# Kernel optimization log

Hardware: AMD Instinct MI355X
Metric: run time of the kernel (lower is better)

The kernel has to match this reference:

```python
import jax, jax.numpy as jnp
import numpy as np

B, T, N, C = 32, 64, 1000, 8
HG, HL, OUT, E = 16, 256, 24, 16000


def setup_inputs() -> dict:
    key = jax.random.key(0)
    ks = jax.random.split(key, 12)
    inp = {
        'x': jax.random.normal(ks[0], (B, T, N, C), jnp.float32),
        'edge_index': jax.random.randint(ks[1], (2, E), 0, N, jnp.int32),
        'edge_weight': jax.random.uniform(ks[2], (E,), jnp.float32),
        # GCNConv params (linear without bias applied before propagate, bias added after)
        'W_gcn': jax.random.normal(ks[3], (C, HG), jnp.float32) * (1.0 / np.sqrt(C)),
        'b_gcn': jnp.zeros((HG,), jnp.float32),
        # single-layer torch LSTM params (gate order i,f,g,o)
        'W_ih': jax.random.normal(ks[4], (4 * HL, N * HG), jnp.float32) * (1.0 / np.sqrt(N * HG)),
        'W_hh': jax.random.normal(ks[5], (4 * HL, HL), jnp.float32) * (1.0 / np.sqrt(HL)),
        'b_ih': jnp.zeros((4 * HL,), jnp.float32),
        'b_hh': jnp.zeros((4 * HL,), jnp.float32),
        'W_proj': jax.random.normal(ks[6], (OUT, HL), jnp.float32) * (1.0 / np.sqrt(HL)),
        'b_proj': jnp.zeros((OUT,), jnp.float32),
    }
    return inp


def reference(x, edge_index, edge_weight, W_gcn, b_gcn, W_ih, W_hh, b_ih, b_hh, W_proj, b_proj):
    b, t, n, c = x.shape
    hg = W_gcn.shape[1]
    row, col = edge_index[0], edge_index[1]

    # --- GCNConv normalization (gcn_norm with self-loops, fill_value=1) ---
    # Edges index only nodes 0..N-1 of the flattened [b*n] node axis, i.e. batch 0
    # (faithful to the original code's batched-flatten bug). Nodes of batch>0 get
    # degree 1 (self-loop only).
    deg0 = jax.ops.segment_sum(edge_weight, col, num_segments=n) + 1.0  # [n]
    dis = deg0 ** -0.5
    norm = dis[row] * edge_weight * dis[col]                            # [E]

    xw = jnp.einsum('btnc,ch->btnh', x, W_gcn)                          # [b,t,n,hg]

    # self-loop contribution: 1/deg for batch 0, identity (deg=1) for batch>0
    inv_deg = jnp.ones((b, n), x.dtype).at[0].set(1.0 / deg0)
    out = xw * inv_deg[:, None, :, None]

    # neighbor aggregation (only batch 0 receives messages)
    msg = norm[None, :, None] * xw[0][:, row, :]                        # [t,E,hg]
    agg0 = jnp.zeros((t, n, hg), x.dtype).at[:, col, :].add(msg)        # [t,n,hg]
    h_gcn = out.at[0].add(agg0) + b_gcn                                 # [b,t,n,hg]

    seq = h_gcn.reshape(b, t, n * hg)

    # --- single-layer LSTM (batch_first), torch gate order i,f,g,o ---
    hl = W_hh.shape[1]
    bias = b_ih + b_hh

    def step(carry, xt):
        h, cc = carry
        gates = xt @ W_ih.T + h @ W_hh.T + bias
        i, f, g, o = jnp.split(gates, 4, axis=-1)
        i, f, o = jax.nn.sigmoid(i), jax.nn.sigmoid(f), jax.nn.sigmoid(o)
        g = jnp.tanh(g)
        cc = f * cc + i * g
        h = o * jnp.tanh(cc)
        return (h, cc), None

    h0 = jnp.zeros((b, hl), x.dtype)
    (h_last, _), _ = jax.lax.scan(step, (h0, h0), seq.transpose(1, 0, 2))

    return h_last @ W_proj.T + b_proj
```

## Files before the change

kernel.cpp:

```cpp
#include <hip/hip_runtime.h>
#include <stdint.h>

#define Bz 32
#define Tz 64
#define Nz 1000
#define Cz 8
#define HGz 16
#define HLz 256
#define OUTz 24
#define Ez 16000
#define K2z 8000
#define Mz 2048
#define G4z 1024
#define NSz 8

using half8  = __attribute__((ext_vector_type(8))) _Float16;
using half4  = __attribute__((ext_vector_type(4))) _Float16;
using floatx4 = __attribute__((ext_vector_type(4))) float;

#define SENT 0x7E7E7E7E7E7E7E7EULL

static const size_t OFF_IDEG   = 4096;
static const size_t OFF_CNT    = 73728;
static const size_t OFF_ROFF   = 77824;
static const size_t OFF_CSRS   = 86016;
static const size_t OFF_CSRW   = 151552;
static const size_t OFF_HLAST  = 217088;
static const size_t OFF_PRE16T = 249856;
static const size_t OFF_WHH16  = 4444160;
static const size_t OFF_HX     = 4968448;
static const size_t OFF_BGC    = 6037504;
static const size_t OFF_XT     = 6041600;
static const size_t OFF_WC     = 38809600;
static const size_t OFF_PRES   = 55193600;
static const size_t WS_NEED    = 88748032;

__device__ __forceinline__ void gl_lds16(const void* g, void* l) {
  __builtin_amdgcn_global_load_lds(
      (__attribute__((address_space(1))) void*)(void*)g,
      (__attribute__((address_space(3))) void*)l, 16, 0, 0);
}

__device__ __forceinline__ float sigm(float x) { return 1.0f / (1.0f + __expf(-x)); }
__device__ __forceinline__ float tanhh(float x) { return 1.0f - 2.0f / (__expf(2.0f * x) + 1.0f); }

__global__ void __launch_bounds__(1024) k_prep(const int* __restrict__ ei,
                                               const float* __restrict__ ew,
                                               float* __restrict__ ideg,
                                               int* __restrict__ cntg,
                                               int* __restrict__ roffg,
                                               int* __restrict__ csrs,
                                               float* __restrict__ csrw) {
  __shared__ float disS[1024];
  __shared__ int   cntS[1024];
  __shared__ int   curS[1024];
  __shared__ int   scanS[1024];
  int tid = threadIdx.x;
  disS[tid] = 1.0f;
  cntS[tid] = 0;
  __syncthreads();
  for (int e = tid; e < Ez; e += 1024) {
    int col = ei[Ez + e];
    atomicAdd(&disS[col], ew[e]);
    atomicAdd(&cntS[col], 1);
  }
  __syncthreads();
  float d = disS[tid];
  float dis = 1.0f / sqrtf(d);
  if (tid < Nz) ideg[tid] = 1.0f / d;
  __syncthreads();
  disS[tid] = dis;
  int v0 = cntS[tid];
  scanS[tid] = v0;
  __syncthreads();
  for (int off = 1; off < 1024; off <<= 1) {
    int v = (tid >= off) ? scanS[tid - off] : 0;
    __syncthreads();
    scanS[tid] += v;
    __syncthreads();
  }
  int excl = scanS[tid] - v0;
  roffg[tid] = excl;
  cntg[tid] = v0;
  curS[tid] = excl;
  __syncthreads();
  for (int e = tid; e < Ez; e += 1024) {
    int row = ei[e], col = ei[Ez + e];
    int p = atomicAdd(&curS[col], 1);
    csrs[p] = row;
    csrw[p] = disS[row] * ew[e] * disS[col];
  }
}

__global__ void __launch_bounds__(256) k_fold(const float* __restrict__ Wih,
                                              const float* __restrict__ Wg,
                                              const float* __restrict__ bg,
                                              _Float16* __restrict__ wc,
                                              float* __restrict__ bgc,
                                              const float* __restrict__ Whh,
                                              _Float16* __restrict__ whh16) {
  __shared__ float wgs[Cz * HGz];
  __shared__ float bgs[HGz];
  __shared__ float red[256];
  int tid = threadIdx.x;
  int j = blockIdx.x;
  if (j >= 1024) {
    size_t i = (size_t)(j - 1024) * 256 + tid;
    float4 a = ((const float4*)Whh)[i * 2];
    float4 b = ((const float4*)Whh)[i * 2 + 1];
    half8 h;
    h[0] = (_Float16)a.x; h[1] = (_Float16)a.y; h[2] = (_Float16)a.z; h[3] = (_Float16)a.w;
    h[4] = (_Float16)b.x; h[5] = (_Float16)b.y; h[6] = (_Float16)b.z; h[7] = (_Float16)b.w;
    ((half8*)whh16)[i] = h;
    return;
  }
  if (tid < Cz * HGz) wgs[tid] = Wg[tid];
  if (tid < HGz) bgs[tid] = bg[tid];
  __syncthreads();
  const float* row = Wih + (size_t)j * (Nz * HGz);
  float bacc = 0.f;
  for (int n = tid; n < Nz; n += 256) {
    const float* p = row + n * HGz;
    float w[16];
    float4 v0 = *(const float4*)p, v1 = *(const float4*)(p + 4);
    float4 v2 = *(const float4*)(p + 8), v3 = *(const float4*)(p + 12);
    w[0]=v0.x; w[1]=v0.y; w[2]=v0.z; w[3]=v0.w;
    w[4]=v1.x; w[5]=v1.y; w[6]=v1.z; w[7]=v1.w;
    w[8]=v2.x; w[9]=v2.y; w[10]=v2.z; w[11]=v2.w;
    w[12]=v3.x; w[13]=v3.y; w[14]=v3.z; w[15]=v3.w;
    half8 o;
#pragma unroll
    for (int c = 0; c < Cz; ++c) {
      float s = 0.f;
#pragma unroll
      for (int h = 0; h < HGz; ++h) s += w[h] * wgs[c * HGz + h];
      o[c] = (_Float16)s;
    }
#pragma unroll
    for (int h = 0; h < HGz; ++h) bacc += w[h] * bgs[h];
    *(half8*)(wc + (size_t)j * K2z + n * Cz) = o;
  }
  red[tid] = bacc;
  __syncthreads();
  for (int off = 128; off > 0; off >>= 1) {
    if (tid < off) red[tid] += red[tid + off];
    __syncthreads();
  }
  if (tid == 0) bgc[j] = red[0];
}

__global__ void k_xt(const float* __restrict__ x, const float* __restrict__ ideg,
                     const int* __restrict__ roff, const int* __restrict__ cnt,
                     const int* __restrict__ csrs, const float* __restrict__ csrw,
                     _Float16* __restrict__ xt) {
  if (blockIdx.x >= 250) {
    size_t i = (size_t)(blockIdx.x - 250) * 256 + threadIdx.x;
    const float* src = x + (size_t)Tz * K2z;
    _Float16* dst = xt + (size_t)Tz * K2z;
    float4 a = ((const float4*)src)[i * 2];
    float4 b = ((const float4*)src)[i * 2 + 1];
    half8 h;
    h[0] = (_Float16)a.x; h[1] = (_Float16)a.y; h[2] = (_Float16)a.z; h[3] = (_Float16)a.w;
    h[4] = (_Float16)b.x; h[5] = (_Float16)b.y; h[6] = (_Float16)b.z; h[7] = (_Float16)b.w;
    ((half8*)dst)[i] = h;
    return;
  }
  int g = blockIdx.x * 256 + threadIdx.x;
  if (g >= Tz * Nz) return;
  int t = g / Nz, n = g % Nz;
  const float* xp = x + (size_t)g * Cz;
  float4 a = *(const float4*)xp, b = *(const float4*)(xp + 4);
  float id = ideg[n];
  float s[8] = {id*a.x, id*a.y, id*a.z, id*a.w, id*b.x, id*b.y, id*b.z, id*b.w};
  int i0 = roff[n], nc = cnt[n];
  for (int i = i0; i < i0 + nc; ++i) {
    int src = csrs[i];
    float wv = csrw[i];
    const float* q = x + ((size_t)t * Nz + src) * Cz;
    float4 u = *(const float4*)q, v = *(const float4*)(q + 4);
    s[0] += wv * u.x; s[1] += wv * u.y; s[2] += wv * u.z; s[3] += wv * u.w;
    s[4] += wv * v.x; s[5] += wv * v.y; s[6] += wv * v.z; s[7] += wv * v.w;
  }
  half8 h;
#pragma unroll
  for (int c = 0; c < 8; ++c) h[c] = (_Float16)s[c];
  *(half8*)(xt + (size_t)t * K2z + n * Cz) = h;
}

__global__ void __launch_bounds__(256) k_gemm(const _Float16* __restrict__ A,
                                              const _Float16* __restrict__ Bm,
                                              _Float16* __restrict__ Cp) {
  __shared__ _Float16 As[128 * 32];
  __shared__ _Float16 Bs[128 * 32];
  const int tid = threadIdx.x;
  const int lane = tid & 63;
  const int wave = tid >> 6;
  const int wm = wave & 1, wn = wave >> 1;
  const int quad = lane >> 4, l15 = lane & 15;
  const size_t tm = (size_t)blockIdx.x * 128;
  const size_t tn = (size_t)blockIdx.y * 128;
  const int k0 = blockIdx.z * 1024;
  const int iters = (blockIdx.z < 7) ? 32 : 26;
  _Float16* Cz_ = Cp + (size_t)blockIdx.z * Mz * G4z;
  const int srow = tid >> 2;
  const int skk = (tid & 3) * 8;
  const _Float16* gA0 = A + (tm + srow) * (size_t)K2z + k0 + skk;
  const _Float16* gA1 = gA0 + 64 * (size_t)K2z;
  const _Float16* gB0 = Bm + (tn + srow) * (size_t)K2z + k0 + skk;
  const _Float16* gB1 = gB0 + 64 * (size_t)K2z;
  _Float16* lA0 = &As[tid * 8];
  _Float16* lA1 = &As[2048 + tid * 8];
  _Float16* lB0 = &Bs[tid * 8];
  _Float16* lB1 = &Bs[2048 + tid * 8];
  floatx4 acc[4][4] = {};
  for (int kt = 0; kt < iters; ++kt) {
    __syncthreads();
    gl_lds16(gA0, lA0);
    gl_lds16(gA1, lA1);
    gl_lds16(gB0, lB0);
    gl_lds16(gB1, lB1);
    gA0 += 32; gA1 += 32; gB0 += 32; gB1 += 32;
    __syncthreads();
    half8 af[4], bf[4];
#pragma unroll
    for (int i = 0; i < 4; ++i)
      af[i] = *(const half8*)&As[(wm * 64 + i * 16 + l15) * 32 + quad * 8];
#pragma unroll
    for (int i = 0; i < 4; ++i)
      bf[i] = *(const half8*)&Bs[(wn * 64 + i * 16 + l15) * 32 + quad * 8];
#pragma unroll
    for (int mi = 0; mi < 4; ++mi)
#pragma unroll
      for (int ni = 0; ni < 4; ++ni)
        acc[mi][ni] = __builtin_amdgcn_mfma_f32_16x16x32_f16(af[mi], bf[ni], acc[mi][ni], 0, 0, 0);
  }
#pragma unroll
  for (int mi = 0; mi < 4; ++mi)
#pragma unroll
    for (int ni = 0; ni < 4; ++ni) {
      size_t r0 = tm + wm * 64 + mi * 16 + quad * 4;
      size_t cc = tn + wn * 64 + ni * 16 + l15;
#pragma unroll
      for (int q = 0; q < 4; ++q) Cz_[(r0 + q) * G4z + cc] = (_Float16)acc[mi][ni][q];
    }
}

__global__ void k_reduce(const _Float16* __restrict__ preS, const float* __restrict__ bih,
                         const float* __restrict__ bhh, const float* __restrict__ bgc,
                         _Float16* __restrict__ preT) {
  int t = blockIdx.x;
  int j = blockIdx.y * 256 + threadIdx.x;
  float bias = bih[j] + bhh[j] + bgc[j];
  float v[32];
#pragma unroll
  for (int b = 0; b < 32; ++b) v[b] = bias;
  for (int s = 0; s < NSz; ++s) {
    const _Float16* base = preS + (size_t)s * Mz * G4z;
#pragma unroll
    for (int b = 0; b < 32; ++b)
      v[b] += (float)base[((size_t)b * Tz + t) * G4z + j];
  }
  half8 h[4];
#pragma unroll
  for (int i = 0; i < 32; ++i) ((_Float16*)h)[i] = (_Float16)v[i];
  half8* op = (half8*)(preT + ((size_t)t * G4z + j) * Bz);
#pragma unroll
  for (int i = 0; i < 4; ++i) op[i] = h[i];
}

__global__ void __launch_bounds__(256) k_lstm4(const _Float16* __restrict__ Whh16,
                                               const _Float16* __restrict__ preT,
                                               unsigned long long* __restrict__ hx,
                                               float* __restrict__ hlast) {
  __shared__ _Float16 Ws[256 * 264];
  __shared__ _Float16 hs[2][16 * 264];
  const int tid = threadIdx.x;
  const int d   = blockIdx.x >> 2;
  const int ws_ = blockIdx.x & 3;
  const int wv = tid >> 6;
  const int lane = tid & 63;
  const int quad = lane >> 4, l15 = lane & 15;

  for (int i = tid; i < 2 * 16 * 264; i += 256) ((_Float16*)hs)[i] = (_Float16)0.f;
#pragma unroll
  for (int rr = 0; rr < 2; ++rr) {
    int rp = (tid >> 1) + rr * 128;
    int g = rp >> 6, hl64 = rp & 63;
    int grow = g * 256 + ws_ * 64 + hl64;
    const half8* src = (const half8*)(Whh16 + (size_t)grow * HLz + (tid & 1) * 128);
    half8* dst = (half8*)&Ws[rp * 264 + (tid & 1) * 128];
#pragma unroll
    for (int u = 0; u < 16; ++u) dst[u] = src[u];
  }
  float cst[4] = {0.f, 0.f, 0.f, 0.f};
  const int hlG = ws_ * 64 + wv * 16 + l15;
  __syncthreads();

  for (int t = 0; t < Tz; ++t) {
    half4 pq[4];
    if (quad == 0) {
#pragma unroll
      for (int g = 0; g < 4; ++g)
        pq[g] = *(const half4*)(preT + ((size_t)t * G4z + g * HLz + hlG) * Bz + d * 4);
    }
    if (t > 0) {
      const unsigned long long* hsrc = hx + ((size_t)d * 65 + t) * 256;
      unsigned long long u;
      while ((u = __hip_atomic_load(hsrc + tid, __ATOMIC_RELAXED,
                                    __HIP_MEMORY_SCOPE_AGENT)) == SENT)
        __builtin_amdgcn_s_sleep(1);
      half4 hv = __builtin_bit_cast(half4, u);
      _Float16* hb = &hs[t & 1][0];
#pragma unroll
      for (int q = 0; q < 4; ++q) hb[q * 264 + tid] = hv[q];
    }
    __syncthreads();
    floatx4 acc[4] = {};
    const _Float16* hrow = &hs[t & 1][0];
#pragma unroll
    for (int kt = 0; kt < 8; ++kt) {
      half8 a = *(const half8*)&hrow[l15 * 264 + kt * 32 + quad * 8];
#pragma unroll
      for (int g = 0; g < 4; ++g) {
        half8 b = *(const half8*)&Ws[(g * 64 + wv * 16 + l15) * 264 + kt * 32 + quad * 8];
        acc[g] = __builtin_amdgcn_mfma_f32_16x16x32_f16(a, b, acc[g], 0, 0, 0);
      }
    }
    if (quad == 0) {
      half4 o;
#pragma unroll
      for (int q = 0; q < 4; ++q) {
        float gi = acc[0][q] + (float)pq[0][q];
        float gf = acc[1][q] + (float)pq[1][q];
        float gg = acc[2][q] + (float)pq[2][q];
        float go = acc[3][q] + (float)pq[3][q];
        float iv = sigm(gi), fv = sigm(gf), gv = tanhh(gg), ov = sigm(go);
        float cn = fv * cst[q] + iv * gv;
        cst[q] = cn;
        float hn = ov * tanhh(cn);
        o[q] = (_Float16)hn;
        if (t == Tz - 1) hlast[(size_t)(d * 4 + q) * HLz + hlG] = hn;
      }
      if (t < Tz - 1) {
        __hip_atomic_store(hx + ((size_t)d * 65 + t + 1) * 256 + hlG,
                           __builtin_bit_cast(unsigned long long, o),
                           __ATOMIC_RELAXED, __HIP_MEMORY_SCOPE_AGENT);
      }
    }
  }
}

__global__ void k_proj(const float* __restrict__ hlast, const float* __restrict__ Wp,
                       const float* __restrict__ bp, float* __restrict__ out) {
  int idx = blockIdx.x * 256 + threadIdx.x;
  if (idx >= Bz * OUTz) return;
  int b = idx / OUTz, o = idx % OUTz;
  const float* h = hlast + (size_t)b * HLz;
  const float* wr = Wp + (size_t)o * HLz;
  float s = 0.f;
  for (int k = 0; k < HLz; k += 4) {
    float4 hv = *(const float4*)&h[k];
    float4 wv = *(const float4*)&wr[k];
    s += hv.x * wv.x + hv.y * wv.y + hv.z * wv.z + hv.w * wv.w;
  }
  out[idx] = s + bp[o];
}

extern "C" void kernel_launch(void* const* d_in, const int* in_sizes, int n_in,
                              void* d_out, int out_size, void* d_ws, size_t ws_size,
                              hipStream_t stream) {
  const float* x   = (const float*)d_in[0];
  const int*   ei  = (const int*)d_in[1];
  const float* ew  = (const float*)d_in[2];
  const float* Wg  = (const float*)d_in[3];
  const float* bg  = (const float*)d_in[4];
  const float* Wih = (const float*)d_in[5];
  const float* Whh = (const float*)d_in[6];
  const float* bih = (const float*)d_in[7];
  const float* bhh = (const float*)d_in[8];
  const float* Wp  = (const float*)d_in[9];
  const float* bp  = (const float*)d_in[10];
  float* out = (float*)d_out;
  char* ws = (char*)d_ws;
  if (ws_size < WS_NEED) return;

  float* ideg  = (float*)(ws + OFF_IDEG);
  int*   cnt   = (int*)(ws + OFF_CNT);
  int*   roff  = (int*)(ws + OFF_ROFF);
  int*   csrs  = (int*)(ws + OFF_CSRS);
  float* csrw  = (float*)(ws + OFF_CSRW);
  float* hlast = (float*)(ws + OFF_HLAST);
  _Float16* preT  = (_Float16*)(ws + OFF_PRE16T);
  _Float16* whh16 = (_Float16*)(ws + OFF_WHH16);
  unsigned long long* hx = (unsigned long long*)(ws + OFF_HX);
  float* bgc   = (float*)(ws + OFF_BGC);
  _Float16* xt    = (_Float16*)(ws + OFF_XT);
  _Float16* wc    = (_Float16*)(ws + OFF_WC);
  _Float16* preS  = (_Float16*)(ws + OFF_PRES);

  hipMemsetAsync(ws + OFF_HX, 0x7E, (size_t)8 * 65 * 256 * 8, stream);

  k_prep<<<1, 1024, 0, stream>>>(ei, ew, ideg, cnt, roff, csrs, csrw);
  k_fold<<<1152, 256, 0, stream>>>(Wih, Wg, bg, wc, bgc, Whh, whh16);
  k_xt<<<8000, 256, 0, stream>>>(x, ideg, roff, cnt, csrs, csrw, xt);
  k_gemm<<<dim3(16, 8, NSz), 256, 0, stream>>>(xt, wc, preS);
  k_reduce<<<dim3(Tz, 4), 256, 0, stream>>>(preS, bih, bhh, bgc, preT);
  k_lstm4<<<32, 256, 0, stream>>>(whh16, preT, hx, hlast);
  k_proj<<<3, 256, 0, stream>>>(hlast, Wp, bp, out);
}
```

Baseline: 456.7 us.

## Split LSTM recurrence across block pairs with half-K overlap and register-held weights

Replaces the 32-block LSTM kernel (4 blocks per 4-batch group, all exchanging h via global memory) with pairs of 512-thread blocks, each covering 16 batch rows and half the hidden units. Each block multiplies its own local half of h before it polls for the partner's half, so part of the MFMA work overlaps the cross-block wait. Half of the W_hh gate tiles are kept in registers to cut LDS traffic. Blocks are spread so only 4 of 16 do work, and each step now needs two block barriers and larger per-block LDS use.

```diff
diff --git a/kernel.cpp b/kernel.cpp
--- a/kernel.cpp
+++ b/kernel.cpp
@@ -268,85 +268,124 @@
   for (int i = 0; i < 4; ++i) op[i] = h[i];
 }
 
-__global__ void __launch_bounds__(256) k_lstm4(const _Float16* __restrict__ Whh16,
+template <int KB>
+__device__ __forceinline__ void mfma_phase(const _Float16* hrow,
+                                           const _Float16* wb0,
+                                           const _Float16* wb1,
+                                           const half8 (&wreg)[2][8],
+                                           floatx4 (&acc)[4]) {
+#pragma unroll
+  for (int kk = 0; kk < 4; ++kk) {
+    const int kt = KB + kk;
+    half8 a  = *(const half8*)(hrow + kt * 32);
+    half8 b0 = *(const half8*)(wb0 + kt * 32);
+    half8 b1 = *(const half8*)(wb1 + kt * 32);
+    acc[0] = __builtin_amdgcn_mfma_f32_16x16x32_f16(a, b0, acc[0], 0, 0, 0);
+    acc[1] = __builtin_amdgcn_mfma_f32_16x16x32_f16(a, b1, acc[1], 0, 0, 0);
+    acc[2] = __builtin_amdgcn_mfma_f32_16x16x32_f16(a, wreg[0][kt], acc[2], 0, 0, 0);
+    acc[3] = __builtin_amdgcn_mfma_f32_16x16x32_f16(a, wreg[1][kt], acc[3], 0, 0, 0);
+  }
+}
+
+__global__ void __launch_bounds__(512) k_lstm2(const _Float16* __restrict__ Whh16,
                                                const _Float16* __restrict__ preT,
                                                unsigned long long* __restrict__ hx,
                                                float* __restrict__ hlast) {
-  __shared__ _Float16 Ws[256 * 264];
-  __shared__ _Float16 hs[2][16 * 264];
+  const int sub = blockIdx.x & 7;
+  if (sub > 1) return;
+  const int bg = sub;
+  const int hh = blockIdx.x >> 3;
+
+  __shared__ _Float16 Ws[8 * 2 * 16 * 264];
+  __shared__ _Float16 hb[2 * 16 * 264];
+
   const int tid = threadIdx.x;
-  const int d   = blockIdx.x >> 2;
-  const int ws_ = blockIdx.x & 3;
-  const int wv = tid >> 6;
+  const int w = tid >> 6;
   const int lane = tid & 63;
   const int quad = lane >> 4, l15 = lane & 15;
 
-  for (int i = tid; i < 2 * 16 * 264; i += 256) ((_Float16*)hs)[i] = (_Float16)0.f;
-#pragma unroll
-  for (int rr = 0; rr < 2; ++rr) {
-    int rp = (tid >> 1) + rr * 128;
-    int g = rp >> 6, hl64 = rp & 63;
-    int grow = g * 256 + ws_ * 64 + hl64;
-    const half8* src = (const half8*)(Whh16 + (size_t)grow * HLz + (tid & 1) * 128);
-    half8* dst = (half8*)&Ws[rp * 264 + (tid & 1) * 128];
-#pragma unroll
-    for (int u = 0; u < 16; ++u) dst[u] = src[u];
-  }
+  for (int i = tid; i < 2 * 16 * 264; i += 512) hb[i] = (_Float16)0.f;
+
+  for (int i = tid; i < 256 * 32; i += 512) {
+    int lr = i >> 5, u = i & 31;
+    int g = lr >> 7, rr = lr & 127;
+    int ww = rr >> 4, r = rr & 15;
+    int grow = g * 256 + hh * 128 + rr;
+    *(half8*)&Ws[(((ww * 2 + g) * 16 + r) * 264) + u * 8] =
+        *(const half8*)(Whh16 + (size_t)grow * 256 + u * 8);
+  }
+  half8 wreg[2][8];
+#pragma unroll
+  for (int g = 0; g < 2; ++g) {
+    const _Float16* src = Whh16 + ((size_t)(g + 2) * 256 + hh * 128 + w * 16 + l15) * 256 + quad * 8;
+#pragma unroll
+    for (int kt = 0; kt < 8; ++kt) wreg[g][kt] = *(const half8*)(src + kt * 32);
+  }
+
+  const int hlL = w * 16 + l15;
+  const int hlG = hh * 128 + hlL;
+  unsigned long long* pubBase = hx + ((size_t)bg * 64 * 2 + hh) * 512 + (size_t)hlL * 4 + quad;
+  const unsigned long long* polBase = hx + ((size_t)bg * 64 * 2 + (hh ^ 1)) * 512 + tid;
+
+  const _Float16* wb0 = &Ws[((w * 2 + 0) * 16 + l15) * 264 + quad * 8];
+  const _Float16* wb1 = &Ws[((w * 2 + 1) * 16 + l15) * 264 + quad * 8];
+
   float cst[4] = {0.f, 0.f, 0.f, 0.f};
-  const int hlG = ws_ * 64 + wv * 16 + l15;
   __syncthreads();
 
   for (int t = 0; t < Tz; ++t) {
+    const int p = t & 1;
     half4 pq[4];
-    if (quad == 0) {
-#pragma unroll
-      for (int g = 0; g < 4; ++g)
-        pq[g] = *(const half4*)(preT + ((size_t)t * G4z + g * HLz + hlG) * Bz + d * 4);
-    }
+    const _Float16* pT = preT + (size_t)t * (G4z * Bz) + bg * 16 + quad * 4;
+#pragma unroll
+    for (int g = 0; g < 4; ++g)
+      pq[g] = *(const half4*)(pT + (size_t)(g * 256 + hlG) * Bz);
+
+    floatx4 acc[4] = {};
+    const _Float16* hrow = &hb[p * (16 * 264) + l15 * 264 + quad * 8];
+
+    if (hh == 0) mfma_phase<0>(hrow, wb0, wb1, wreg, acc);
+    else         mfma_phase<4>(hrow, wb0, wb1, wreg, acc);
+
     if (t > 0) {
-      const unsigned long long* hsrc = hx + ((size_t)d * 65 + t) * 256;
+      const unsigned long long* src = polBase + (size_t)t * 1024;
       unsigned long long u;
-      while ((u = __hip_atomic_load(hsrc + tid, __ATOMIC_RELAXED,
-                                    __HIP_MEMORY_SCOPE_AGENT)) == SENT)
+      while ((u = __hip_atomic_load(src, __ATOMIC_RELAXED, __HIP_MEMORY_SCOPE_AGENT)) == SENT)
         __builtin_amdgcn_s_sleep(1);
       half4 hv = __builtin_bit_cast(half4, u);
-      _Float16* hb = &hs[t & 1][0];
-#pragma unroll
-      for (int q = 0; q < 4; ++q) hb[q * 264 + tid] = hv[q];
+      const int phl = tid >> 2, pbh = tid & 3;
+      _Float16* dst = &hb[p * (16 * 264) + (pbh * 4) * 264 + ((hh ^ 1) * 128 + phl)];
+#pragma unroll
+      for (int q = 0; q < 4; ++q) dst[q * 264] = hv[q];
     }
     __syncthreads();
-    floatx4 acc[4] = {};
-    const _Float16* hrow = &hs[t & 1][0];
-#pragma unroll
-    for (int kt = 0; kt < 8; ++kt) {
-      half8 a = *(const half8*)&hrow[l15 * 264 + kt * 32 + quad * 8];
-#pragma unroll
-      for (int g = 0; g < 4; ++g) {
-        half8 b = *(const half8*)&Ws[(g * 64 + wv * 16 + l15) * 264 + kt * 32 + quad * 8];
-        acc[g] = __builtin_amdgcn_mfma_f32_16x16x32_f16(a, b, acc[g], 0, 0, 0);
-      }
+
+    if (hh == 0) mfma_phase<4>(hrow, wb0, wb1, wreg, acc);
+    else         mfma_phase<0>(hrow, wb0, wb1, wreg, acc);
+
+    half4 o4;
+#pragma unroll
+    for (int q = 0; q < 4; ++q) {
+      float gi = acc[0][q] + (float)pq[0][q];
+      float gf = acc[1][q] + (float)pq[1][q];
+      float gg = acc[2][q] + (float)pq[2][q];
+      float go = acc[3][q] + (float)pq[3][q];
+      float iv = sigm(gi), fv = sigm(gf), gv = tanhh(gg), ov = sigm(go);
+      float cn = fv * cst[q] + iv * gv;
+      cst[q] = cn;
+      float hn = ov * tanhh(cn);
+      o4[q] = (_Float16)hn;
+      if (t == Tz - 1) hlast[(size_t)(bg * 16 + quad * 4 + q) * HLz + hlG] = hn;
     }
-    if (quad == 0) {
-      half4 o;
-#pragma unroll
-      for (int q = 0; q < 4; ++q) {
-        float gi = acc[0][q] + (float)pq[0][q];
-        float gf = acc[1][q] + (float)pq[1][q];
-        float gg = acc[2][q] + (float)pq[2][q];
-        float go = acc[3][q] + (float)pq[3][q];
-        float iv = sigm(gi), fv = sigm(gf), gv = tanhh(gg), ov = sigm(go);
-        float cn = fv * cst[q] + iv * gv;
-        cst[q] = cn;
-        float hn = ov * tanhh(cn);
-        o[q] = (_Float16)hn;
-        if (t == Tz - 1) hlast[(size_t)(d * 4 + q) * HLz + hlG] = hn;
-      }
-      if (t < Tz - 1) {
-        __hip_atomic_store(hx + ((size_t)d * 65 + t + 1) * 256 + hlG,
-                           __builtin_bit_cast(unsigned long long, o),
-                           __ATOMIC_RELAXED, __HIP_MEMORY_SCOPE_AGENT);
-      }
+    if (t < Tz - 1) {
+      __hip_atomic_store(pubBase + (size_t)(t + 1) * 1024,
+                         __builtin_bit_cast(unsigned long long, o4),
+                         __ATOMIC_RELAXED, __HIP_MEMORY_SCOPE_AGENT);
+      _Float16* dst = &hb[(p ^ 1) * (16 * 264) + (quad * 4) * 264 + hlG];
+#pragma unroll
+      for (int q = 0; q < 4; ++q) dst[q * 264] = o4[q];
     }
+    __syncthreads();
   }
 }
 
@@ -398,13 +437,13 @@
   _Float16* wc    = (_Float16*)(ws + OFF_WC);
   _Float16* preS  = (_Float16*)(ws + OFF_PRES);
 
-  hipMemsetAsync(ws + OFF_HX, 0x7E, (size_t)8 * 65 * 256 * 8, stream);
+  hipMemsetAsync(ws + OFF_HX, 0x7E, (size_t)2 * 64 * 2 * 128 * 4 * 8, stream);
 
   k_prep<<<1, 1024, 0, stream>>>(ei, ew, ideg, cnt, roff, csrs, csrw);
   k_fold<<<1152, 256, 0, stream>>>(Wih, Wg, bg, wc, bgc, Whh, whh16);
   k_xt<<<8000, 256, 0, stream>>>(x, ideg, roff, cnt, csrs, csrw, xt);
   k_gemm<<<dim3(16, 8, NSz), 256, 0, stream>>>(xt, wc, preS);
   k_reduce<<<dim3(Tz, 4), 256, 0, stream>>>(preS, bih, bhh, bgc, preT);
-  k_lstm4<<<32, 256, 0, stream>>>(whh16, preT, hx, hlast);
+  k_lstm2<<<16, 512, 0, stream>>>(whh16, preT, hx, hlast);
   k_proj<<<3, 256, 0, stream>>>(hlast, Wp, bp, out);
 }
```

New measurement: 494.4 us. +8.2%, slower.

## Replace cross-block LSTM recurrence with per-batch-group single-block LSTM

Applied to the files above, without the earlier changes.

The LSTM recurrence used to run across 32 blocks that exchanged hidden-state slices through global-memory spin-waits on sentinel values every timestep. Each of two 512-thread blocks now owns 16 batch rows and holds all of W_hh itself: three gates' slices live in registers and the output gate's slice in LDS. The hidden state is exchanged through a double-buffered LDS buffer with one __syncthreads per step. This removes the global handshakes and the hx sentinel memset, and preT's layout is changed to match. The cost is that only 2 CUs do the serial recurrence, with heavy register pressure (48 half8 per thread) and more MFMA work per block.

```diff
diff --git a/kernel.cpp b/kernel.cpp
--- a/kernel.cpp
+++ b/kernel.cpp
@@ -18,8 +18,6 @@
 using half4  = __attribute__((ext_vector_type(4))) _Float16;
 using floatx4 = __attribute__((ext_vector_type(4))) float;
 
-#define SENT 0x7E7E7E7E7E7E7E7EULL
-
 static const size_t OFF_IDEG   = 4096;
 static const size_t OFF_CNT    = 73728;
 static const size_t OFF_ROFF   = 77824;
@@ -28,7 +26,6 @@
 static const size_t OFF_HLAST  = 217088;
 static const size_t OFF_PRE16T = 249856;
 static const size_t OFF_WHH16  = 4444160;
-static const size_t OFF_HX     = 4968448;
 static const size_t OFF_BGC    = 6037504;
 static const size_t OFF_XT     = 6041600;
 static const size_t OFF_WC     = 38809600;
@@ -260,93 +257,103 @@
     for (int b = 0; b < 32; ++b)
       v[b] += (float)base[((size_t)b * Tz + t) * G4z + j];
   }
-  half8 h[4];
-#pragma unroll
-  for (int i = 0; i < 32; ++i) ((_Float16*)h)[i] = (_Float16)v[i];
-  half8* op = (half8*)(preT + ((size_t)t * G4z + j) * Bz);
-#pragma unroll
-  for (int i = 0; i < 4; ++i) op[i] = h[i];
-}
-
-__global__ void __launch_bounds__(256) k_lstm4(const _Float16* __restrict__ Whh16,
-                                               const _Float16* __restrict__ preT,
-                                               unsigned long long* __restrict__ hx,
-                                               float* __restrict__ hlast) {
-  __shared__ _Float16 Ws[256 * 264];
-  __shared__ _Float16 hs[2][16 * 264];
+#pragma unroll
+  for (int b = 0; b < 32; ++b)
+    preT[((size_t)t * 32 + b) * G4z + j] = (_Float16)v[b];
+}
+
+__global__ void __launch_bounds__(512, 2) k_lstm1(const _Float16* __restrict__ Whh16,
+                                                  const _Float16* __restrict__ preT,
+                                                  float* __restrict__ hlast) {
+  __shared__ _Float16 Wl[8][2][16 * 264];
+  __shared__ _Float16 hb[2][16 * 264];
   const int tid = threadIdx.x;
-  const int d   = blockIdx.x >> 2;
-  const int ws_ = blockIdx.x & 3;
-  const int wv = tid >> 6;
+  const int w = tid >> 6;
   const int lane = tid & 63;
   const int quad = lane >> 4, l15 = lane & 15;
-
-  for (int i = tid; i < 2 * 16 * 264; i += 256) ((_Float16*)hs)[i] = (_Float16)0.f;
-#pragma unroll
-  for (int rr = 0; rr < 2; ++rr) {
-    int rp = (tid >> 1) + rr * 128;
-    int g = rp >> 6, hl64 = rp & 63;
-    int grow = g * 256 + ws_ * 64 + hl64;
-    const half8* src = (const half8*)(Whh16 + (size_t)grow * HLz + (tid & 1) * 128);
-    half8* dst = (half8*)&Ws[rp * 264 + (tid & 1) * 128];
-#pragma unroll
-    for (int u = 0; u < 16; ++u) dst[u] = src[u];
-  }
-  float cst[4] = {0.f, 0.f, 0.f, 0.f};
-  const int hlG = ws_ * 64 + wv * 16 + l15;
+  const int bg = blockIdx.x;
+
+  for (int i = tid; i < 2 * 16 * 264; i += 512) ((_Float16*)hb)[i] = (_Float16)0.f;
+
+  {
+    const int r = lane >> 2, c4 = lane & 3;
+#pragma unroll
+    for (int ht = 0; ht < 2; ++ht) {
+      const half8* src = (const half8*)(Whh16 + ((size_t)(768 + w * 32 + ht * 16 + r)) * 256 + c4 * 64);
+      half8* dst = (half8*)&Wl[w][ht][r * 264 + c4 * 64];
+#pragma unroll
+      for (int u = 0; u < 8; ++u) dst[u] = src[u];
+    }
+  }
+  half8 wr[6][8];
+#pragma unroll
+  for (int gh = 0; gh < 6; ++gh) {
+    const int g = gh >> 1, ht = gh & 1;
+    const _Float16* src = Whh16 + ((size_t)(g * 256 + w * 32 + ht * 16 + l15)) * 256 + quad * 8;
+#pragma unroll
+    for (int kt = 0; kt < 8; ++kt) wr[gh][kt] = *(const half8*)(src + kt * 32);
+  }
+
+  float cst[2][4] = {{0.f, 0.f, 0.f, 0.f}, {0.f, 0.f, 0.f, 0.f}};
   __syncthreads();
 
   for (int t = 0; t < Tz; ++t) {
-    half4 pq[4];
-    if (quad == 0) {
+    const int p = t & 1;
+    floatx4 acc[8];
+    {
+      const _Float16* pb = preT + ((size_t)t * 32 + bg * 16 + l15) * G4z + w * 32 + quad * 4;
 #pragma unroll
       for (int g = 0; g < 4; ++g)
-        pq[g] = *(const half4*)(preT + ((size_t)t * G4z + g * HLz + hlG) * Bz + d * 4);
-    }
-    if (t > 0) {
-      const unsigned long long* hsrc = hx + ((size_t)d * 65 + t) * 256;
-      unsigned long long u;
-      while ((u = __hip_atomic_load(hsrc + tid, __ATOMIC_RELAXED,
-                                    __HIP_MEMORY_SCOPE_AGENT)) == SENT)
-        __builtin_amdgcn_s_sleep(1);
-      half4 hv = __builtin_bit_cast(half4, u);
-      _Float16* hb = &hs[t & 1][0];
-#pragma unroll
-      for (int q = 0; q < 4; ++q) hb[q * 264 + tid] = hv[q];
-    }
-    __syncthreads();
-    floatx4 acc[4] = {};
-    const _Float16* hrow = &hs[t & 1][0];
+#pragma unroll
+        for (int ht = 0; ht < 2; ++ht) {
+          half4 v = *(const half4*)(pb + g * 256 + ht * 16);
+          floatx4 a;
+          a[0] = (float)v[0]; a[1] = (float)v[1]; a[2] = (float)v[2]; a[3] = (float)v[3];
+          acc[g * 2 + ht] = a;
+        }
+    }
+    const _Float16* hrow = &hb[p][l15 * 264 + quad * 8];
+    const _Float16* wl0 = &Wl[w][0][l15 * 264 + quad * 8];
+    const _Float16* wl1 = &Wl[w][1][l15 * 264 + quad * 8];
 #pragma unroll
     for (int kt = 0; kt < 8; ++kt) {
-      half8 a = *(const half8*)&hrow[l15 * 264 + kt * 32 + quad * 8];
-#pragma unroll
-      for (int g = 0; g < 4; ++g) {
-        half8 b = *(const half8*)&Ws[(g * 64 + wv * 16 + l15) * 264 + kt * 32 + quad * 8];
-        acc[g] = __builtin_amdgcn_mfma_f32_16x16x32_f16(a, b, acc[g], 0, 0, 0);
+      half8 h8 = *(const half8*)(hrow + kt * 32);
+      half8 o0 = *(const half8*)(wl0 + kt * 32);
+      half8 o1 = *(const half8*)(wl1 + kt * 32);
+      acc[0] = __builtin_amdgcn_mfma_f32_16x16x32_f16(wr[0][kt], h8, acc[0], 0, 0, 0);
+      acc[1] = __builtin_amdgcn_mfma_f32_16x16x32_f16(wr[1][kt], h8, acc[1], 0, 0, 0);
+      acc[2] = __builtin_amdgcn_mfma_f32_16x16x32_f16(wr[2][kt], h8, acc[2], 0, 0, 0);
+      acc[3] = __builtin_amdgcn_mfma_f32_16x16x32_f16(wr[3][kt], h8, acc[3], 0, 0, 0);
+      acc[4] = __builtin_amdgcn_mfma_f32_16x16x32_f16(wr[4][kt], h8, acc[4], 0, 0, 0);
+      acc[5] = __builtin_amdgcn_mfma_f32_16x16x32_f16(wr[5][kt], h8, acc[5], 0, 0, 0);
+      acc[6] = __builtin_amdgcn_mfma_f32_16x16x32_f16(o0, h8, acc[6], 0, 0, 0);
+      acc[7] = __builtin_amdgcn_mfma_f32_16x16x32_f16(o1, h8, acc[7], 0, 0, 0);
+    }
+    _Float16* hn_base = &hb[p ^ 1][l15 * 264 + w * 32 + quad * 4];
+#pragma unroll
+    for (int ht = 0; ht < 2; ++ht) {
+      half4 ho;
+      float hf[4];
+#pragma unroll
+      for (int q = 0; q < 4; ++q) {
+        float gi = acc[0 * 2 + ht][q];
+        float gf = acc[1 * 2 + ht][q];
+        float gg = acc[2 * 2 + ht][q];
+        float go = acc[6 + ht][q];
+        float iv = sigm(gi), fv = sigm(gf), gv = tanhh(gg), ov = sigm(go);
+        float cn = fv * cst[ht][q] + iv * gv;
+        cst[ht][q] = cn;
+        float hnv = ov * tanhh(cn);
+        ho[q] = (_Float16)hnv;
+        hf[q] = hnv;
       }
-    }
-    if (quad == 0) {
-      half4 o;
-#pragma unroll
-      for (int q = 0; q < 4; ++q) {
-        float gi = acc[0][q] + (float)pq[0][q];
-        float gf = acc[1][q] + (float)pq[1][q];
-        float gg = acc[2][q] + (float)pq[2][q];
-        float go = acc[3][q] + (float)pq[3][q];
-        float iv = sigm(gi), fv = sigm(gf), gv = tanhh(gg), ov = sigm(go);
-        float cn = fv * cst[q] + iv * gv;
-        cst[q] = cn;
-        float hn = ov * tanhh(cn);
-        o[q] = (_Float16)hn;
-        if (t == Tz - 1) hlast[(size_t)(d * 4 + q) * HLz + hlG] = hn;
+      *(half4*)(hn_base + ht * 16) = ho;
+      if (t == Tz - 1) {
+        float4 o4; o4.x = hf[0]; o4.y = hf[1]; o4.z = hf[2]; o4.w = hf[3];
+        *(float4*)&hlast[(size_t)(bg * 16 + l15) * HLz + w * 32 + ht * 16 + quad * 4] = o4;
       }
-      if (t < Tz - 1) {
-        __hip_atomic_store(hx + ((size_t)d * 65 + t + 1) * 256 + hlG,
-                           __builtin_bit_cast(unsigned long long, o),
-                           __ATOMIC_RELAXED, __HIP_MEMORY_SCOPE_AGENT);
-      }
-    }
+    }
+    __syncthreads();
   }
 }
 
@@ -392,19 +399,16 @@
   float* hlast = (float*)(ws + OFF_HLAST);
   _Float16* preT  = (_Float16*)(ws + OFF_PRE16T);
   _Float16* whh16 = (_Float16*)(ws + OFF_WHH16);
-  unsigned long long* hx = (unsigned long long*)(ws + OFF_HX);
   float* bgc   = (float*)(ws + OFF_BGC);
   _Float16* xt    = (_Float16*)(ws + OFF_XT);
   _Float16* wc    = (_Float16*)(ws + OFF_WC);
   _Float16* preS  = (_Float16*)(ws + OFF_PRES);
-
-  hipMemsetAsync(ws + OFF_HX, 0x7E, (size_t)8 * 65 * 256 * 8, stream);
 
   k_prep<<<1, 1024, 0, stream>>>(ei, ew, ideg, cnt, roff, csrs, csrw);
   k_fold<<<1152, 256, 0, stream>>>(Wih, Wg, bg, wc, bgc, Whh, whh16);
   k_xt<<<8000, 256, 0, stream>>>(x, ideg, roff, cnt, csrs, csrw, xt);
   k_gemm<<<dim3(16, 8, NSz), 256, 0, stream>>>(xt, wc, preS);
   k_reduce<<<dim3(Tz, 4), 256, 0, stream>>>(preS, bih, bhh, bgc, preT);
-  k_lstm4<<<32, 256, 0, stream>>>(whh16, preT, hx, hlast);
+  k_lstm1<<<2, 512, 0, stream>>>(whh16, preT, hlast);
   k_proj<<<3, 256, 0, stream>>>(hlast, Wp, bp, out);
 }
```

New measurement: 626.6 us. 1.37x slower.

## Restructure LSTM recurrence into 2 batch domains with register-resident gate-interleaved weights

Applied to the files above, without the earlier changes.

The recurrent LSTM kernel is reorganized. Instead of 8 batch groups of 4 blocks each holding W_hh in LDS, it now runs 2 batch domains of 8 blocks each, and every wave keeps its slice of W_hh in registers. W_hh is stored permuted so the i,f,g,o gates for each hidden unit are adjacent, and preT is re-laid out to match, so one MFMA output tile carries all four gates. Blocks exchange h through a new hx layout, polling only the slices produced by other blocks and writing their own slice straight to LDS. This is meant to cut LDS traffic and per-step cross-block synchronization cost, but it runs fewer blocks, each with more work, and a more complex exchange pattern.

```diff
diff --git a/kernel.cpp b/kernel.cpp
--- a/kernel.cpp
+++ b/kernel.cpp
@@ -106,12 +106,14 @@
   int j = blockIdx.x;
   if (j >= 1024) {
     size_t i = (size_t)(j - 1024) * 256 + tid;
+    int row = (int)(i >> 5), c8 = (int)(i & 31);
+    int rp = ((row & 255) << 2) | (row >> 8);
     float4 a = ((const float4*)Whh)[i * 2];
     float4 b = ((const float4*)Whh)[i * 2 + 1];
     half8 h;
     h[0] = (_Float16)a.x; h[1] = (_Float16)a.y; h[2] = (_Float16)a.z; h[3] = (_Float16)a.w;
     h[4] = (_Float16)b.x; h[5] = (_Float16)b.y; h[6] = (_Float16)b.z; h[7] = (_Float16)b.w;
-    ((half8*)whh16)[i] = h;
+    ((half8*)whh16)[(size_t)rp * 32 + c8] = h;
     return;
   }
   if (tid < Cz * HGz) wgs[tid] = Wg[tid];
@@ -260,92 +262,107 @@
     for (int b = 0; b < 32; ++b)
       v[b] += (float)base[((size_t)b * Tz + t) * G4z + j];
   }
-  half8 h[4];
-#pragma unroll
-  for (int i = 0; i < 32; ++i) ((_Float16*)h)[i] = (_Float16)v[i];
-  half8* op = (half8*)(preT + ((size_t)t * G4z + j) * Bz);
-#pragma unroll
-  for (int i = 0; i < 4; ++i) op[i] = h[i];
-}
-
-__global__ void __launch_bounds__(256) k_lstm4(const _Float16* __restrict__ Whh16,
-                                               const _Float16* __restrict__ preT,
-                                               unsigned long long* __restrict__ hx,
-                                               float* __restrict__ hlast) {
-  __shared__ _Float16 Ws[256 * 264];
-  __shared__ _Float16 hs[2][16 * 264];
+#pragma unroll
+  for (int b = 0; b < 32; ++b)
+    preT[((size_t)t * 32 + b) * G4z + threadIdx.x * 4 + blockIdx.y] = (_Float16)v[b];
+}
+
+__global__ void __launch_bounds__(256, 1) k_lstmZ(const _Float16* __restrict__ Wp16,
+                                                  const _Float16* __restrict__ preT,
+                                                  unsigned long long* __restrict__ hx,
+                                                  float* __restrict__ hlast) {
+  __shared__ _Float16 hb[2][16 * 264];
   const int tid = threadIdx.x;
-  const int d   = blockIdx.x >> 2;
-  const int ws_ = blockIdx.x & 3;
-  const int wv = tid >> 6;
+  const int w = tid >> 6;
   const int lane = tid & 63;
   const int quad = lane >> 4, l15 = lane & 15;
-
-  for (int i = tid; i < 2 * 16 * 264; i += 256) ((_Float16*)hs)[i] = (_Float16)0.f;
-#pragma unroll
-  for (int rr = 0; rr < 2; ++rr) {
-    int rp = (tid >> 1) + rr * 128;
-    int g = rp >> 6, hl64 = rp & 63;
-    int grow = g * 256 + ws_ * 64 + hl64;
-    const half8* src = (const half8*)(Whh16 + (size_t)grow * HLz + (tid & 1) * 128);
-    half8* dst = (half8*)&Ws[rp * 264 + (tid & 1) * 128];
-#pragma unroll
-    for (int u = 0; u < 16; ++u) dst[u] = src[u];
-  }
-  float cst[4] = {0.f, 0.f, 0.f, 0.f};
-  const int hlG = ws_ * 64 + wv * 16 + l15;
+  const int dom = blockIdx.x >> 3;
+  const int s = blockIdx.x & 7;
+
+  for (int i = tid; i < 2 * 16 * 264; i += 256) ((_Float16*)hb)[i] = (_Float16)0.f;
+
+  half8 wr0[8], wr1[8];
+  {
+    const _Float16* s0 = Wp16 + (size_t)(s * 128 + w * 32 + l15) * 256 + quad * 8;
+    const _Float16* s1 = s0 + 16 * 256;
+#pragma unroll
+    for (int kt = 0; kt < 8; ++kt) { wr0[kt] = *(const half8*)(s0 + kt * 32); }
+#pragma unroll
+    for (int kt = 0; kt < 8; ++kt) { wr1[kt] = *(const half8*)(s1 + kt * 32); }
+  }
+  const int hl0 = s * 32 + w * 8 + quad;
+  const int hl1 = hl0 + 4;
+  const int bl = tid >> 4, hq = tid & 15;
+  const bool dopoll = (hq >> 1) != s;
+  const int bg = dom * 16;
+
+  float cs0 = 0.f, cs1 = 0.f;
   __syncthreads();
 
   for (int t = 0; t < Tz; ++t) {
-    half4 pq[4];
-    if (quad == 0) {
-#pragma unroll
-      for (int g = 0; g < 4; ++g)
-        pq[g] = *(const half4*)(preT + ((size_t)t * G4z + g * HLz + hlG) * Bz + d * 4);
-    }
-    if (t > 0) {
-      const unsigned long long* hsrc = hx + ((size_t)d * 65 + t) * 256;
-      unsigned long long u;
-      while ((u = __hip_atomic_load(hsrc + tid, __ATOMIC_RELAXED,
-                                    __HIP_MEMORY_SCOPE_AGENT)) == SENT)
-        __builtin_amdgcn_s_sleep(1);
-      half4 hv = __builtin_bit_cast(half4, u);
-      _Float16* hb = &hs[t & 1][0];
-#pragma unroll
-      for (int q = 0; q < 4; ++q) hb[q * 264 + tid] = hv[q];
-    }
-    __syncthreads();
-    floatx4 acc[4] = {};
-    const _Float16* hrow = &hs[t & 1][0];
+    const _Float16* pp = preT + ((size_t)t * 32 + bg + l15) * G4z;
+    half4 pq0 = *(const half4*)(pp + hl0 * 4);
+    half4 pq1 = *(const half4*)(pp + hl1 * 4);
+
+    if (t > 0 && dopoll) {
+      const unsigned long long* src = hx + (((size_t)dom * 64 + t) * 16 + bl) * 64 + hq * 4;
+      unsigned long long* dst = (unsigned long long*)&hb[t & 1][bl * 264 + hq * 16];
+#pragma unroll
+      for (int w4 = 0; w4 < 4; ++w4) {
+        unsigned long long v;
+        while ((v = __hip_atomic_load(src + w4, __ATOMIC_RELAXED,
+                                      __HIP_MEMORY_SCOPE_AGENT)) == SENT)
+          __builtin_amdgcn_s_sleep(2);
+        dst[w4] = v;
+      }
+    }
+    __syncthreads();
+
+    floatx4 a0, a1;
+    a0[0] = (float)pq0[0]; a0[1] = (float)pq0[1]; a0[2] = (float)pq0[2]; a0[3] = (float)pq0[3];
+    a1[0] = (float)pq1[0]; a1[1] = (float)pq1[1]; a1[2] = (float)pq1[2]; a1[3] = (float)pq1[3];
+    const _Float16* hrow = &hb[t & 1][l15 * 264 + quad * 8];
 #pragma unroll
     for (int kt = 0; kt < 8; ++kt) {
-      half8 a = *(const half8*)&hrow[l15 * 264 + kt * 32 + quad * 8];
-#pragma unroll
-      for (int g = 0; g < 4; ++g) {
-        half8 b = *(const half8*)&Ws[(g * 64 + wv * 16 + l15) * 264 + kt * 32 + quad * 8];
-        acc[g] = __builtin_amdgcn_mfma_f32_16x16x32_f16(a, b, acc[g], 0, 0, 0);
+      half8 h8 = *(const half8*)(hrow + kt * 32);
+      a0 = __builtin_amdgcn_mfma_f32_16x16x32_f16(wr0[kt], h8, a0, 0, 0, 0);
+      a1 = __builtin_amdgcn_mfma_f32_16x16x32_f16(wr1[kt], h8, a1, 0, 0, 0);
+    }
+    unsigned short u0, u1;
+    {
+      float iv = sigm(a0[0]), fv = sigm(a0[1]), gv = tanhh(a0[2]), ov = sigm(a0[3]);
+      float cn = fv * cs0 + iv * gv; cs0 = cn;
+      float hn = ov * tanhh(cn);
+      u0 = __builtin_bit_cast(unsigned short, (_Float16)hn);
+      if (t == Tz - 1) hlast[(size_t)(bg + l15) * HLz + hl0] = hn;
+    }
+    {
+      float iv = sigm(a1[0]), fv = sigm(a1[1]), gv = tanhh(a1[2]), ov = sigm(a1[3]);
+      float cn = fv * cs1 + iv * gv; cs1 = cn;
+      float hn = ov * tanhh(cn);
+      u1 = __builtin_bit_cast(unsigned short, (_Float16)hn);
+      if (t == Tz - 1) hlast[(size_t)(bg + l15) * HLz + hl1] = hn;
+    }
+    if (t < Tz - 1) {
+      int i0 = u0, i1 = u1;
+      int g01 = __shfl(i0, l15 + 16, 64), g02 = __shfl(i0, l15 + 32, 64), g03 = __shfl(i0, l15 + 48, 64);
+      int g11 = __shfl(i1, l15 + 16, 64), g12 = __shfl(i1, l15 + 32, 64), g13 = __shfl(i1, l15 + 48, 64);
+      if (quad == 0) {
+        unsigned long long v0 = (unsigned long long)(unsigned short)i0 |
+                                ((unsigned long long)(unsigned short)g01 << 16) |
+                                ((unsigned long long)(unsigned short)g02 << 32) |
+                                ((unsigned long long)(unsigned short)g03 << 48);
+        unsigned long long v1 = (unsigned long long)(unsigned short)i1 |
+                                ((unsigned long long)(unsigned short)g11 << 16) |
+                                ((unsigned long long)(unsigned short)g12 << 32) |
+                                ((unsigned long long)(unsigned short)g13 << 48);
+        unsigned long long* pb = hx + (((size_t)dom * 64 + t + 1) * 16 + l15) * 64 + s * 8 + w * 2;
+        __hip_atomic_store(pb, v0, __ATOMIC_RELAXED, __HIP_MEMORY_SCOPE_AGENT);
+        __hip_atomic_store(pb + 1, v1, __ATOMIC_RELAXED, __HIP_MEMORY_SCOPE_AGENT);
       }
-    }
-    if (quad == 0) {
-      half4 o;
-#pragma unroll
-      for (int q = 0; q < 4; ++q) {
-        float gi = acc[0][q] + (float)pq[0][q];
-        float gf = acc[1][q] + (float)pq[1][q];
-        float gg = acc[2][q] + (float)pq[2][q];
-        float go = acc[3][q] + (float)pq[3][q];
-        float iv = sigm(gi), fv = sigm(gf), gv = tanhh(gg), ov = sigm(go);
-        float cn = fv * cst[q] + iv * gv;
-        cst[q] = cn;
-        float hn = ov * tanhh(cn);
-        o[q] = (_Float16)hn;
-        if (t == Tz - 1) hlast[(size_t)(d * 4 + q) * HLz + hlG] = hn;
-      }
-      if (t < Tz - 1) {
-        __hip_atomic_store(hx + ((size_t)d * 65 + t + 1) * 256 + hlG,
-                           __builtin_bit_cast(unsigned long long, o),
-                           __ATOMIC_RELAXED, __HIP_MEMORY_SCOPE_AGENT);
-      }
+      _Float16* hbn = &hb[(t + 1) & 1][l15 * 264];
+      hbn[hl0] = __builtin_bit_cast(_Float16, u0);
+      hbn[hl1] = __builtin_bit_cast(_Float16, u1);
     }
   }
 }
@@ -398,13 +415,13 @@
   _Float16* wc    = (_Float16*)(ws + OFF_WC);
   _Float16* preS  = (_Float16*)(ws + OFF_PRES);
 
-  hipMemsetAsync(ws + OFF_HX, 0x7E, (size_t)8 * 65 * 256 * 8, stream);
+  hipMemsetAsync(ws + OFF_HX, 0x7E, (size_t)2 * 64 * 16 * 64 * 8, stream);
 
   k_prep<<<1, 1024, 0, stream>>>(ei, ew, ideg, cnt, roff, csrs, csrw);
   k_fold<<<1152, 256, 0, stream>>>(Wih, Wg, bg, wc, bgc, Whh, whh16);
   k_xt<<<8000, 256, 0, stream>>>(x, ideg, roff, cnt, csrs, csrw, xt);
   k_gemm<<<dim3(16, 8, NSz), 256, 0, stream>>>(xt, wc, preS);
   k_reduce<<<dim3(Tz, 4), 256, 0, stream>>>(preS, bih, bhh, bgc, preT);
-  k_lstm4<<<32, 256, 0, stream>>>(whh16, preT, hx, hlast);
+  k_lstmZ<<<16, 256, 0, stream>>>(whh16, preT, hx, hlast);
   k_proj<<<3, 256, 0, stream>>>(hlast, Wp, bp, out);
 }
```

Measured after the change: 456.9 us. No clear change (+0.0%).
